# Optimization experiments

Hardware: AMD Instinct MI355X
Metric: run time of the kernel (lower is better)

Reference implementation:

```python
import math
import jax, jax.numpy as jnp
import numpy as np

N, C, T, V = 256, 128, 64, 25
OUT, H = 128, 4
D = OUT // H  # 32
MAX_LEN = 64
KSIZE = 9
EPS = 1e-5
NEG = -1e9


def setup_inputs() -> dict:
    key = jax.random.key(0)
    ks = jax.random.split(key, 20)
    std = 0.02
    return {
        "x": jax.random.normal(ks[0], (N, C, T, V), jnp.float32),
        # BatchNorm (eval mode) on input
        "bn_gamma": 1.0 + 0.1 * jax.random.normal(ks[1], (C,), jnp.float32),
        "bn_beta": 0.1 * jax.random.normal(ks[2], (C,), jnp.float32),
        "bn_mean": 0.1 * jax.random.normal(ks[3], (C,), jnp.float32),
        "bn_var": jax.random.uniform(ks[4], (C,), jnp.float32, 0.5, 1.5),
        # 1x1 convs (qkv_kernel=1)
        "qk_w": std * jax.random.normal(ks[5], (2 * OUT, C), jnp.float32),
        "qk_b": std * jax.random.normal(ks[6], (2 * OUT,), jnp.float32),
        "v_w": std * jax.random.normal(ks[7], (OUT, C), jnp.float32),
        "v_b": std * jax.random.normal(ks[8], (OUT,), jnp.float32),
        "logit_scale": jnp.full((H, 1, 1), math.log(math.sqrt(D)), jnp.float32),
        "rel_pos_bias": std * jax.random.normal(ks[9], (H, 2 * MAX_LEN - 1), jnp.float32),
        "proj_w": std * jax.random.normal(ks[10], (OUT, OUT), jnp.float32),
        "proj_b": std * jax.random.normal(ks[11], (OUT,), jnp.float32),
        # output BatchNorm (eval mode)
        "bno_gamma": 1.0 + 0.1 * jax.random.normal(ks[12], (OUT,), jnp.float32),
        "bno_beta": 0.1 * jax.random.normal(ks[13], (OUT,), jnp.float32),
        "bno_mean": 0.1 * jax.random.normal(ks[14], (OUT,), jnp.float32),
        "bno_var": jax.random.uniform(ks[15], (OUT,), jnp.float32, 0.5, 1.5),
    }


def _bn(x, gamma, beta, mean, var):
    # eval-mode BatchNorm2d over channel dim of (N, C, T, V)
    inv = gamma / jnp.sqrt(var + EPS)
    return (x - mean[:, None, None]) * inv[:, None, None] + beta[:, None, None]


def reference(x, bn_gamma, bn_beta, bn_mean, bn_var, qk_w, qk_b, v_w, v_b,
              logit_scale, rel_pos_bias, proj_w, proj_b,
              bno_gamma, bno_beta, bno_mean, bno_var):
    n, c, t, v = x.shape
    x_in = x
    xb = _bn(x, bn_gamma, bn_beta, bn_mean, bn_var)

    # 1x1 conv qk: (n, 2*OUT, t, v) -> split into q, k of shape (n, v, h, t, d)
    qk = jnp.einsum('nctv,oc->notv', xb, qk_w) + qk_b[:, None, None]
    qk = qk.reshape(n, 2, H, D, t, v).transpose(1, 0, 5, 2, 4, 3)  # (2, n, v, h, t, d)
    q, k = qk[0], qk[1]
    val = (jnp.einsum('nctv,oc->notv', xb, v_w) + v_b[:, None, None])
    val = val.reshape(n, H, D, t, v).transpose(0, 4, 1, 3, 2)  # (n, v, h, t, d)

    # cosine-sim attention: L2-normalize q, k; learned per-head temperature
    scale = jnp.exp(jnp.minimum(logit_scale, math.log(100.0)))  # (h,1,1)
    q = q / jnp.maximum(jnp.linalg.norm(q, axis=-1, keepdims=True), 1e-12) * scale
    k = k / jnp.maximum(jnp.linalg.norm(k, axis=-1, keepdims=True), 1e-12)

    # SDPA applies an extra 1/sqrt(d) scale by default
    scores = jnp.einsum('nvhid,nvhjd->nvhij', q, k) / math.sqrt(D)

    coords = jnp.arange(t)
    rel_idx = coords[None, :] - coords[:, None] + (MAX_LEN - 1)  # (t, t)
    bias = rel_pos_bias[:, rel_idx]  # (h, t, t)
    local = jnp.abs(coords[:, None] - coords[None, :]) <= KSIZE // 2  # (t, t)

    scores = jnp.where(local[None, None, None], scores + bias[None, None], NEG)
    attn = jax.nn.softmax(scores, axis=-1)
    out = jnp.einsum('nvhij,nvhjd->nvhid', attn, val)  # (n, v, h, t, d)
    out = out.transpose(0, 2, 4, 3, 1).reshape(n, OUT, t, v)

    out = jnp.einsum('nctv,oc->notv', out, proj_w) + proj_b[:, None, None] + x_in
    # stride=1 -> pool is identity; ffn_ratio=0 -> no FFN; dropout=0
    out = _bn(out, bno_gamma, bno_beta, bno_mean, bno_var)
    return out
```

## Files before the change

### kernel.cpp

```cpp
#include <hip/hip_runtime.h>
#include <hip/hip_bf16.h>

typedef __attribute__((ext_vector_type(8))) short bf16x8;
typedef __attribute__((ext_vector_type(4))) float f32x4;

static __device__ __forceinline__ unsigned short f2bf(float f){
  __hip_bfloat16 h = __float2bfloat16(f);
  return __builtin_bit_cast(unsigned short, h);
}
static __device__ __forceinline__ unsigned int pk2(float a, float b){
  return (unsigned int)f2bf(a) | ((unsigned int)f2bf(b) << 16);
}
static __device__ __forceinline__ float bf2f(unsigned short h){
  return __uint_as_float(((unsigned int)h) << 16);
}
static __device__ __forceinline__ f32x4 mfma16(bf16x8 a, bf16x8 b, f32x4 c){
  return __builtin_amdgcn_mfma_f32_16x16x32_bf16(a, b, c, 0, 0, 0);
}

__global__ void prep_kernel(
    const float* __restrict__ bn_g, const float* __restrict__ bn_b,
    const float* __restrict__ bn_m, const float* __restrict__ bn_v,
    const float* __restrict__ qk_w, const float* __restrict__ qk_b,
    const float* __restrict__ v_w,  const float* __restrict__ v_b,
    const float* __restrict__ ls,   const float* __restrict__ proj_w,
    const float* __restrict__ proj_b,
    const float* __restrict__ bo_g, const float* __restrict__ bo_b,
    const float* __restrict__ bo_m, const float* __restrict__ bo_v,
    unsigned short* __restrict__ Wqkv, unsigned short* __restrict__ Wp,
    float* __restrict__ bqf, float* __restrict__ bpf,
    float* __restrict__ rsf, float* __restrict__ shf)
{
  int g = blockIdx.x * 256 + threadIdx.x;
  if (g < 384){
    const float* wr = (g < 256) ? (qk_w + g * 128) : (v_w + (g - 256) * 128);
    float acc = (g < 256) ? qk_b[g] : v_b[g - 256];
    for (int c = 0; c < 128; c++){
      float inv = bn_g[c] * rsqrtf(bn_v[c] + 1e-5f);
      float sh  = bn_b[c] - bn_m[c] * inv;
      float wv  = wr[c];
      Wqkv[g * 128 + c] = f2bf(wv * inv);
      acc += wv * sh;
    }
    bqf[g] = acc;
  } else if (g < 512){
    int o = g - 384;
    float invo = bo_g[o] * rsqrtf(bo_v[o] + 1e-5f);
    for (int c = 0; c < 128; c++)
      Wp[o * 128 + c] = f2bf(proj_w[o * 128 + c] * invo);
    bpf[o] = (proj_b[o] - bo_m[o]) * invo + bo_b[o];
    rsf[o] = invo;
    if (o < 4)
      shf[o] = expf(fminf(ls[o], 4.6051701859880914f)) * 0.17677669529663687f;
  }
}

__global__ __launch_bounds__(256) void pack_x(const float* __restrict__ x,
                                              unsigned short* __restrict__ xb)
{
  __shared__ __align__(16) unsigned short tile[200][136];
  int n = blockIdx.x >> 3;
  int slab = blockIdx.x & 7;
  int t0 = slab * 8;
  int tid = threadIdx.x;
  const float* xn = x + (long)n * 204800 + (long)t0 * 25;
  #pragma unroll 5
  for (int k = 0; k < 25; k++){
    int idx = tid + k * 256;
    int c  = idx / 50;
    int r4 = idx - c * 50;
    float4 f = *((const float4*)(xn + (long)c * 1600 + r4 * 4));
    tile[r4*4+0][c] = f2bf(f.x);
    tile[r4*4+1][c] = f2bf(f.y);
    tile[r4*4+2][c] = f2bf(f.z);
    tile[r4*4+3][c] = f2bf(f.w);
  }
  __syncthreads();
  for (int k = 0; k < 13; k++){
    int idx = tid + k * 256;
    if (idx < 3200){
      int r  = idx >> 4;
      int u  = idx & 15;
      int lt = r / 25;
      int vv = r - lt * 25;
      int c0 = (u ^ lt) * 8;
      uint4 d = *((const uint4*)&tile[r][c0]);
      *((uint4*)(xb + ((long)(n * 25 + vv) * 64 + t0 + lt) * 128 + u * 8)) = d;
    }
  }
}

__global__ __launch_bounds__(256) void unpack_out(const unsigned short* __restrict__ ob,
                                                  float* __restrict__ out)
{
  __shared__ __align__(16) unsigned short tile[200][136];
  int n = blockIdx.x >> 3;
  int slab = blockIdx.x & 7;
  int t0 = slab * 8;
  int tid = threadIdx.x;
  for (int k = 0; k < 13; k++){
    int idx = tid + k * 256;
    if (idx < 3200){
      int r  = idx >> 4;
      int u  = idx & 15;
      int lt = r / 25;
      int vv = r - lt * 25;
      uint4 d = *((const uint4*)(ob + ((long)(n * 25 + vv) * 64 + t0 + lt) * 128 + u * 8));
      int c0 = (u ^ lt) * 8;
      *((uint4*)&tile[r][c0]) = d;
    }
  }
  __syncthreads();
  float* on = out + (long)n * 204800 + (long)t0 * 25;
  #pragma unroll 5
  for (int k = 0; k < 25; k++){
    int idx = tid + k * 256;
    int c  = idx / 50;
    int r4 = idx - c * 50;
    float4 f;
    f.x = bf2f(tile[r4*4+0][c]);
    f.y = bf2f(tile[r4*4+1][c]);
    f.z = bf2f(tile[r4*4+2][c]);
    f.w = bf2f(tile[r4*4+3][c]);
    *((float4*)(on + (long)c * 1600 + r4 * 4)) = f;
  }
}

#define B_X     0
#define B_R1    16384
#define B_VT    57344
#define B_BQ    74752
#define B_BP    76288
#define B_RS    76800
#define B_SH    77312
#define B_BIAS  77328
#define B_TOTAL 79360

__global__ __launch_bounds__(256, 2) void fused_compute(
    const unsigned short* __restrict__ xb,
    const unsigned short* __restrict__ Wqkv,
    const unsigned short* __restrict__ Wp,
    const float* __restrict__ bqf,
    const float* __restrict__ bpf,
    const float* __restrict__ rsf,
    const float* __restrict__ shf,
    const float* __restrict__ relb,
    unsigned short* __restrict__ ob)
{
  __shared__ __align__(16) char smem[B_TOTAL];
  unsigned short* xl   = (unsigned short*)(smem + B_X);
  unsigned short* r1   = (unsigned short*)(smem + B_R1);
  unsigned short* vT   = (unsigned short*)(smem + B_VT);
  float* c_bq   = (float*)(smem + B_BQ);
  float* c_bp   = (float*)(smem + B_BP);
  float* c_rs   = (float*)(smem + B_RS);
  float* c_sh   = (float*)(smem + B_SH);
  float* c_bias = (float*)(smem + B_BIAS);

  int bid = blockIdx.x;
  int swz = (bid & 7) * 800 + (bid >> 3);
  long tileoff = (long)swz * 8192;
  int tid  = threadIdx.x;
  int lane = tid & 63;
  int w    = tid >> 6;
  int h    = w;
  int l4   = lane >> 4;
  int l15  = lane & 15;

  for (int i = tid; i < 384; i += 256) c_bq[i] = bqf[i];
  if (tid < 128){ c_bp[tid] = bpf[tid]; c_rs[tid] = rsf[tid]; }
  if (tid < 4) c_sh[tid] = shf[tid];
  for (int i = tid; i < 508; i += 256) c_bias[i] = relb[i];
  {
    const uint4* src = (const uint4*)(xb + tileoff);
    uint4* dst = (uint4*)xl;
    #pragma unroll
    for (int i = 0; i < 4; i++) dst[tid + i * 256] = src[tid + i * 256];
  }
  __syncthreads();

  const f32x4 zero4 = {0.f, 0.f, 0.f, 0.f};

  unsigned short* qlds = r1 + h * 5120;
  unsigned short* klds = qlds + 2560;
  {
    int rowbase[6] = {32*h, 32*h + 16, 128 + 32*h, 128 + 32*h + 16,
                      256 + 32*h, 256 + 32*h + 16};
    f32x4 acc[6][4];
    #pragma unroll
    for (int m = 0; m < 6; m++)
      #pragma unroll
      for (int nt = 0; nt < 4; nt++) acc[m][nt] = zero4;
    #pragma unroll
    for (int ks = 0; ks < 4; ks++){
      int ko = ks * 32 + l4 * 8;
      bf16x8 a[6], b[4];
      #pragma unroll
      for (int m = 0; m < 6; m++)
        a[m] = *((const bf16x8*)(Wqkv + (rowbase[m] + l15) * 128 + ko));
      #pragma unroll
      for (int nt = 0; nt < 4; nt++){
        int row = nt * 16 + l15;
        b[nt] = *((const bf16x8*)((const char*)xl + row * 256 + ((ko * 2) ^ ((row & 7) << 4))));
      }
      #pragma unroll
      for (int m = 0; m < 6; m++)
        #pragma unroll
        for (int nt = 0; nt < 4; nt++)
          acc[m][nt] = mfma16(a[m], b[nt], acc[m][nt]);
    }
    #pragma unroll
    for (int m = 0; m < 6; m++)
      #pragma unroll
      for (int nt = 0; nt < 4; nt++)
        #pragma unroll
        for (int r = 0; r < 4; r++)
          acc[m][nt][r] += c_bq[rowbase[m] + l4 * 4 + r];

    float scq[4], sck[4];
    #pragma unroll
    for (int nt = 0; nt < 4; nt++){
      float ssq = 0.f, ssk = 0.f;
      #pragma unroll
      for (int r = 0; r < 4; r++){
        ssq += acc[0][nt][r] * acc[0][nt][r] + acc[1][nt][r] * acc[1][nt][r];
        ssk += acc[2][nt][r] * acc[2][nt][r] + acc[3][nt][r] * acc[3][nt][r];
      }
      ssq += __shfl_xor(ssq, 16); ssq += __shfl_xor(ssq, 32);
      ssk += __shfl_xor(ssk, 16); ssk += __shfl_xor(ssk, 32);
      scq[nt] = c_sh[h] / fmaxf(sqrtf(ssq), 1e-12f);
      sck[nt] = 1.0f   / fmaxf(sqrtf(ssk), 1e-12f);
    }
    #pragma unroll
    for (int m = 0; m < 2; m++)
      #pragma unroll
      for (int nt = 0; nt < 4; nt++){
        uint2 p;
        p.x = pk2(acc[m][nt][0] * scq[nt], acc[m][nt][1] * scq[nt]);
        p.y = pk2(acc[m][nt][2] * scq[nt], acc[m][nt][3] * scq[nt]);
        *((uint2*)&qlds[(nt * 16 + l15) * 40 + m * 16 + l4 * 4]) = p;
      }
    #pragma unroll
    for (int m = 2; m < 4; m++)
      #pragma unroll
      for (int nt = 0; nt < 4; nt++){
        uint2 p;
        p.x = pk2(acc[m][nt][0] * sck[nt], acc[m][nt][1] * sck[nt]);
        p.y = pk2(acc[m][nt][2] * sck[nt], acc[m][nt][3] * sck[nt]);
        *((uint2*)&klds[(nt * 16 + l15) * 40 + (m - 2) * 16 + l4 * 4]) = p;
      }
    #pragma unroll
    for (int m = 4; m < 6; m++)
      #pragma unroll
      for (int nt = 0; nt < 4; nt++)
        #pragma unroll
        for (int r = 0; r < 4; r++)
          vT[(h * 32 + (m - 4) * 16 + l4 * 4 + r) * 68 + nt * 16 + l15] = f2bf(acc[m][nt][r]);
  }
  __builtin_amdgcn_sched_barrier(0);

  bf16x8 kf[4], qf[4];
  {
    int ko = l4 * 8;
    #pragma unroll
    for (int jt = 0; jt < 4; jt++)
      kf[jt] = *((const bf16x8*)&klds[(jt * 16 + l15) * 40 + ko]);
    #pragma unroll
    for (int it = 0; it < 4; it++)
      qf[it] = *((const bf16x8*)&qlds[(it * 16 + l15) * 40 + ko]);
  }
  __builtin_amdgcn_sched_barrier(0);

  unsigned short* attn = r1 + h * 5120;
  {
    f32x4 sAcc[4][4];
    #pragma unroll
    for (int jt = 0; jt < 4; jt++)
      #pragma unroll
      for (int it = 0; it < 4; it++) sAcc[jt][it] = zero4;
    #pragma unroll
    for (int jt = 0; jt < 4; jt++)
      #pragma unroll
      for (int it = 0; it < 4; it++)
        sAcc[jt][it] = mfma16(kf[jt], qf[it], sAcc[jt][it]);

    #pragma unroll
    for (int it = 0; it < 4; it++){
      int i = it * 16 + l15;
      float sv[16];
      float mx = -1e30f;
      #pragma unroll
      for (int jt = 0; jt < 4; jt++){
        #pragma unroll
        for (int r = 0; r < 4; r++){
          int j = jt * 16 + l4 * 4 + r;
          int rel = j - i;
          float s;
          if (rel < -4 || rel > 4) s = -1e9f;
          else s = sAcc[jt][it][r] + c_bias[h * 127 + rel + 63];
          sv[jt * 4 + r] = s;
          mx = fmaxf(mx, s);
        }
      }
      mx = fmaxf(mx, __shfl_xor(mx, 16));
      mx = fmaxf(mx, __shfl_xor(mx, 32));
      float sum = 0.f;
      #pragma unroll
      for (int k2 = 0; k2 < 16; k2++){
        float p = __expf(sv[k2] - mx);
        sv[k2] = p; sum += p;
      }
      sum += __shfl_xor(sum, 16);
      sum += __shfl_xor(sum, 32);
      float rs = 1.0f / sum;
      #pragma unroll
      for (int jt = 0; jt < 4; jt++){
        uint2 p;
        p.x = pk2(sv[jt*4+0] * rs, sv[jt*4+1] * rs);
        p.y = pk2(sv[jt*4+2] * rs, sv[jt*4+3] * rs);
        *((uint2*)&attn[i * 72 + jt * 16 + l4 * 4]) = p;
      }
    }
  }
  __builtin_amdgcn_sched_barrier(0);

  bf16x8 av[2][2], bv2[4][2];
  {
    int ko = l4 * 8;
    #pragma unroll
    for (int mt = 0; mt < 2; mt++)
      #pragma unroll
      for (int ks2 = 0; ks2 < 2; ks2++)
        av[mt][ks2] = *((const bf16x8*)&vT[(h * 32 + mt * 16 + l15) * 68 + ks2 * 32 + ko]);
    #pragma unroll
    for (int it = 0; it < 4; it++)
      #pragma unroll
      for (int ks2 = 0; ks2 < 2; ks2++)
        bv2[it][ks2] = *((const bf16x8*)&attn[(it * 16 + l15) * 72 + ks2 * 32 + ko]);
  }
  __syncthreads();

  unsigned short* ao = r1;
  {
    f32x4 pAcc[2][4];
    #pragma unroll
    for (int mt = 0; mt < 2; mt++)
      #pragma unroll
      for (int it = 0; it < 4; it++) pAcc[mt][it] = zero4;
    #pragma unroll
    for (int mt = 0; mt < 2; mt++)
      #pragma unroll
      for (int it = 0; it < 4; it++)
        #pragma unroll
        for (int ks2 = 0; ks2 < 2; ks2++)
          pAcc[mt][it] = mfma16(av[mt][ks2], bv2[it][ks2], pAcc[mt][it]);
    #pragma unroll
    for (int mt = 0; mt < 2; mt++)
      #pragma unroll
      for (int it = 0; it < 4; it++){
        int d0 = mt * 16 + l4 * 4;
        int i  = it * 16 + l15;
        uint2 p;
        p.x = pk2(pAcc[mt][it][0], pAcc[mt][it][1]);
        p.y = pk2(pAcc[mt][it][2], pAcc[mt][it][3]);
        *((uint2*)&ao[i * 136 + h * 32 + d0]) = p;
      }
  }
  __syncthreads();

  {
    f32x4 acc2[2][4];
    #pragma unroll
    for (int mt = 0; mt < 2; mt++)
      #pragma unroll
      for (int nt = 0; nt < 4; nt++) acc2[mt][nt] = zero4;
    #pragma unroll
    for (int ks = 0; ks < 4; ks++){
      int ko = ks * 32 + l4 * 8;
      bf16x8 a2[2], b2[4];
      #pragma unroll
      for (int mt = 0; mt < 2; mt++)
        a2[mt] = *((const bf16x8*)(Wp + (w * 32 + mt * 16 + l15) * 128 + ko));
      #pragma unroll
      for (int nt = 0; nt < 4; nt++)
        b2[nt] = *((const bf16x8*)&ao[(nt * 16 + l15) * 136 + ko]);
      #pragma unroll
      for (int mt = 0; mt < 2; mt++)
        #pragma unroll
        for (int nt = 0; nt < 4; nt++)
          acc2[mt][nt] = mfma16(a2[mt], b2[nt], acc2[mt][nt]);
    }
    #pragma unroll
    for (int mt = 0; mt < 2; mt++)
      #pragma unroll
      for (int nt = 0; nt < 4; nt++){
        int o0 = w * 32 + mt * 16 + l4 * 4;
        int t2 = nt * 16 + l15;
        char* cell = (char*)xl + t2 * 256 + ((o0 * 2) ^ ((t2 & 7) << 4));
        uint2 resid = *((const uint2*)cell);
        float r0 = bf2f((unsigned short)(resid.x & 0xFFFFu));
        float r1f = bf2f((unsigned short)(resid.x >> 16));
        float r2 = bf2f((unsigned short)(resid.y & 0xFFFFu));
        float r3 = bf2f((unsigned short)(resid.y >> 16));
        uint2 p;
        p.x = pk2(acc2[mt][nt][0] + c_bp[o0+0] + r0 * c_rs[o0+0],
                  acc2[mt][nt][1] + c_bp[o0+1] + r1f * c_rs[o0+1]);
        p.y = pk2(acc2[mt][nt][2] + c_bp[o0+2] + r2 * c_rs[o0+2],
                  acc2[mt][nt][3] + c_bp[o0+3] + r3 * c_rs[o0+3]);
        *((uint2*)cell) = p;
      }
  }
  __syncthreads();
  {
    const uint4* sxl = (const uint4*)xl;
    uint4* obt = (uint4*)(ob + tileoff);
    #pragma unroll
    for (int i = 0; i < 4; i++) obt[tid + i * 256] = sxl[tid + i * 256];
  }
}

#define F_X     0
#define F_RB    17408
#define F_VT    58368
#define F_BQ    76800
#define F_BP    78336
#define F_RS    78848
#define F_SH    79360
#define F_BIAS  79376
#define F_TOTAL 81408

__global__ __launch_bounds__(256, 2) void fused_scatter(
    const float* __restrict__ x,
    const unsigned short* __restrict__ Wqkv,
    const unsigned short* __restrict__ Wp,
    const float* __restrict__ bqf,
    const float* __restrict__ bpf,
    const float* __restrict__ rsf,
    const float* __restrict__ shf,
    const float* __restrict__ relb,
    float* __restrict__ out)
{
  __shared__ __align__(16) char smem[F_TOTAL];
  unsigned short* xl   = (unsigned short*)(smem + F_X);
  unsigned short* rbu  = (unsigned short*)(smem + F_RB);
  unsigned short* vT   = (unsigned short*)(smem + F_VT);
  float* c_bq   = (float*)(smem + F_BQ);
  float* c_bp   = (float*)(smem + F_BP);
  float* c_rs   = (float*)(smem + F_RS);
  float* c_sh   = (float*)(smem + F_SH);
  float* c_bias = (float*)(smem + F_BIAS);

  int bid = blockIdx.x;
  int swz = (bid & 7) * 800 + (bid >> 3);
  int n = swz / 25;
  int v = swz - n * 25;
  int tid  = threadIdx.x;
  int lane = tid & 63;
  int w    = tid >> 6;
  int l4   = lane >> 4;
  int l15  = lane & 15;

  for (int i = tid; i < 384; i += 256) c_bq[i] = bqf[i];
  if (tid < 128){ c_bp[tid] = bpf[tid]; c_rs[tid] = rsf[tid]; }
  if (tid < 4) c_sh[tid] = shf[tid];
  for (int i = tid; i < 508; i += 256) c_bias[i] = relb[i];

  {
    const float* xb2 = x + (long)n * 204800 + v;
    int t  = lane;
    int cg = w * 32;
    #pragma unroll
    for (int i = 0; i < 4; i++){
      unsigned int pk[4];
      #pragma unroll
      for (int e = 0; e < 4; e++){
        int c = cg + i * 8 + e * 2;
        pk[e] = pk2(xb2[(long)c * 1600 + t * 25], xb2[(long)(c + 1) * 1600 + t * 25]);
      }
      uint4 q4; q4.x = pk[0]; q4.y = pk[1]; q4.z = pk[2]; q4.w = pk[3];
      *((uint4*)&xl[t * 136 + cg + i * 8]) = q4;
    }
  }
  __syncthreads();

  const f32x4 zero4 = {0.f, 0.f, 0.f, 0.f};

  {
    f32x4 acc[6][4];
    #pragma unroll
    for (int m = 0; m < 6; m++)
      #pragma unroll
      for (int nt = 0; nt < 4; nt++) acc[m][nt] = zero4;
    int Mb = w * 96;
    #pragma unroll
    for (int ks = 0; ks < 4; ks++){
      int ko = ks * 32 + l4 * 8;
      bf16x8 a[6], b[4];
      #pragma unroll
      for (int m = 0; m < 6; m++)
        a[m] = *((const bf16x8*)(Wqkv + (Mb + m * 16 + l15) * 128 + ko));
      #pragma unroll
      for (int nt = 0; nt < 4; nt++)
        b[nt] = *((const bf16x8*)&xl[(nt * 16 + l15) * 136 + ko]);
      #pragma unroll
      for (int m = 0; m < 6; m++)
        #pragma unroll
        for (int nt = 0; nt < 4; nt++)
          acc[m][nt] = mfma16(a[m], b[nt], acc[m][nt]);
    }
    #pragma unroll
    for (int m = 0; m < 6; m++){
      #pragma unroll
      for (int nt = 0; nt < 4; nt++){
        #pragma unroll
        for (int r = 0; r < 4; r++){
          int o  = Mb + m * 16 + l4 * 4 + r;
          int t2 = nt * 16 + l15;
          unsigned short bv = f2bf(acc[m][nt][r] + c_bq[o]);
          if (o < 256){
            rbu[(((o >> 7) * 4 + ((o >> 5) & 3)) * 64 + t2) * 40 + (o & 31)] = bv;
          } else {
            vT[(o - 256) * 72 + t2] = bv;
          }
        }
      }
    }
  }
  __syncthreads();

  {
    #pragma unroll
    for (int rr = 0; rr < 2; rr++){
      int r = tid + rr * 256;
      unsigned short* row = &rbu[r * 40];
      uint4 u0 = *((uint4*)(row + 0));
      uint4 u1 = *((uint4*)(row + 8));
      uint4 u2 = *((uint4*)(row + 16));
      uint4 u3 = *((uint4*)(row + 24));
      unsigned int uu[16] = {u0.x,u0.y,u0.z,u0.w, u1.x,u1.y,u1.z,u1.w,
                             u2.x,u2.y,u2.z,u2.w, u3.x,u3.y,u3.z,u3.w};
      float vals[32];
      float ss = 0.f;
      #pragma unroll
      for (int k2 = 0; k2 < 16; k2++){
        float f0 = bf2f((unsigned short)(uu[k2] & 0xFFFFu));
        float f1 = bf2f((unsigned short)(uu[k2] >> 16));
        vals[2*k2] = f0; vals[2*k2+1] = f1;
        ss += f0 * f0 + f1 * f1;
      }
      float sc = 1.0f / fmaxf(sqrtf(ss), 1e-12f);
      if (r < 256) sc *= c_sh[(r >> 6) & 3];
      #pragma unroll
      for (int k2 = 0; k2 < 16; k2++)
        uu[k2] = pk2(vals[2*k2] * sc, vals[2*k2+1] * sc);
      u0.x=uu[0];u0.y=uu[1];u0.z=uu[2];u0.w=uu[3];
      u1.x=uu[4];u1.y=uu[5];u1.z=uu[6];u1.w=uu[7];
      u2.x=uu[8];u2.y=uu[9];u2.z=uu[10];u2.w=uu[11];
      u3.x=uu[12];u3.y=uu[13];u3.z=uu[14];u3.w=uu[15];
      *((uint4*)(row + 0))  = u0;
      *((uint4*)(row + 8))  = u1;
      *((uint4*)(row + 16)) = u2;
      *((uint4*)(row + 24)) = u3;
    }
  }
  __syncthreads();

  int h = w;
  bf16x8 kf[4], qf[4];
  {
    const unsigned short* kb = &rbu[(256 + h * 64) * 40];
    const unsigned short* qb = &rbu[(h * 64) * 40];
    int ko = l4 * 8;
    #pragma unroll
    for (int jt = 0; jt < 4; jt++)
      kf[jt] = *((const bf16x8*)(kb + (jt * 16 + l15) * 40 + ko));
    #pragma unroll
    for (int it = 0; it < 4; it++)
      qf[it] = *((const bf16x8*)(qb + (it * 16 + l15) * 40 + ko));
  }
  __syncthreads();

  unsigned short* attn = rbu + h * 4608;
  {
    f32x4 sAcc[4][4];
    #pragma unroll
    for (int jt = 0; jt < 4; jt++)
      #pragma unroll
      for (int it = 0; it < 4; it++) sAcc[jt][it] = zero4;
    #pragma unroll
    for (int jt = 0; jt < 4; jt++)
      #pragma unroll
      for (int it = 0; it < 4; it++)
        sAcc[jt][it] = mfma16(kf[jt], qf[it], sAcc[jt][it]);

    #pragma unroll
    for (int it = 0; it < 4; it++){
      int i = it * 16 + l15;
      float sv[16];
      float mx = -1e30f;
      #pragma unroll
      for (int jt = 0; jt < 4; jt++){
        #pragma unroll
        for (int r = 0; r < 4; r++){
          int j = jt * 16 + l4 * 4 + r;
          int rel = j - i;
          float s;
          if (rel < -4 || rel > 4) s = -1e9f;
          else s = sAcc[jt][it][r] + c_bias[h * 127 + rel + 63];
          sv[jt * 4 + r] = s;
          mx = fmaxf(mx, s);
        }
      }
      mx = fmaxf(mx, __shfl_xor(mx, 16));
      mx = fmaxf(mx, __shfl_xor(mx, 32));
      float sum = 0.f;
      #pragma unroll
      for (int k2 = 0; k2 < 16; k2++){
        float p = __expf(sv[k2] - mx);
        sv[k2] = p; sum += p;
      }
      sum += __shfl_xor(sum, 16);
      sum += __shfl_xor(sum, 32);
      float rs = 1.0f / sum;
      #pragma unroll
      for (int jt = 0; jt < 4; jt++)
        #pragma unroll
        for (int r = 0; r < 4; r++)
          attn[i * 72 + (jt * 16 + l4 * 4 + r)] = f2bf(sv[jt * 4 + r] * rs);
    }
  }

  bf16x8 av[2][2], bv2[4][2];
  {
    int ko = l4 * 8;
    #pragma unroll
    for (int mt = 0; mt < 2; mt++)
      #pragma unroll
      for (int ks2 = 0; ks2 < 2; ks2++)
        av[mt][ks2] = *((const bf16x8*)&vT[(h * 32 + mt * 16 + l15) * 72 + ks2 * 32 + ko]);
    #pragma unroll
    for (int it = 0; it < 4; it++)
      #pragma unroll
      for (int ks2 = 0; ks2 < 2; ks2++)
        bv2[it][ks2] = *((const bf16x8*)&attn[(it * 16 + l15) * 72 + ks2 * 32 + ko]);
  }
  __syncthreads();

  unsigned short* ao = rbu;
  {
    f32x4 pAcc[2][4];
    #pragma unroll
    for (int mt = 0; mt < 2; mt++)
      #pragma unroll
      for (int it = 0; it < 4; it++) pAcc[mt][it] = zero4;
    #pragma unroll
    for (int mt = 0; mt < 2; mt++)
      #pragma unroll
      for (int it = 0; it < 4; it++)
        #pragma unroll
        for (int ks2 = 0; ks2 < 2; ks2++)
          pAcc[mt][it] = mfma16(av[mt][ks2], bv2[it][ks2], pAcc[mt][it]);
    #pragma unroll
    for (int mt = 0; mt < 2; mt++)
      #pragma unroll
      for (int it = 0; it < 4; it++)
        #pragma unroll
        for (int r = 0; r < 4; r++){
          int d = mt * 16 + l4 * 4 + r;
          int i = it * 16 + l15;
          ao[i * 136 + h * 32 + d] = f2bf(pAcc[mt][it][r]);
        }
  }
  __syncthreads();

  {
    f32x4 acc2[2][4];
    #pragma unroll
    for (int mt = 0; mt < 2; mt++)
      #pragma unroll
      for (int nt = 0; nt < 4; nt++) acc2[mt][nt] = zero4;
    #pragma unroll
    for (int ks = 0; ks < 4; ks++){
      int ko = ks * 32 + l4 * 8;
      bf16x8 a2[2], b2[4];
      #pragma unroll
      for (int mt = 0; mt < 2; mt++)
        a2[mt] = *((const bf16x8*)(Wp + (w * 32 + mt * 16 + l15) * 128 + ko));
      #pragma unroll
      for (int nt = 0; nt < 4; nt++)
        b2[nt] = *((const bf16x8*)&ao[(nt * 16 + l15) * 136 + ko]);
      #pragma unroll
      for (int mt = 0; mt < 2; mt++)
        #pragma unroll
        for (int nt = 0; nt < 4; nt++)
          acc2[mt][nt] = mfma16(a2[mt], b2[nt], acc2[mt][nt]);
    }
    float* outp = out + (long)n * 204800 + v;
    #pragma unroll
    for (int mt = 0; mt < 2; mt++)
      #pragma unroll
      for (int nt = 0; nt < 4; nt++)
        #pragma unroll
        for (int r = 0; r < 4; r++){
          int o  = w * 32 + mt * 16 + l4 * 4 + r;
          int t2 = nt * 16 + l15;
          float val = acc2[mt][nt][r] + c_bp[o] + bf2f(xl[t2 * 136 + o]) * c_rs[o];
          outp[(long)o * 1600 + t2 * 25] = val;
        }
  }
}

extern "C" void kernel_launch(void* const* d_in, const int* in_sizes, int n_in,
                              void* d_out, int out_size, void* d_ws, size_t ws_size,
                              hipStream_t stream)
{
  const float* x     = (const float*)d_in[0];
  const float* bn_g  = (const float*)d_in[1];
  const float* bn_b  = (const float*)d_in[2];
  const float* bn_m  = (const float*)d_in[3];
  const float* bn_v  = (const float*)d_in[4];
  const float* qk_w  = (const float*)d_in[5];
  const float* qk_b  = (const float*)d_in[6];
  const float* v_w   = (const float*)d_in[7];
  const float* v_b   = (const float*)d_in[8];
  const float* ls    = (const float*)d_in[9];
  const float* relb  = (const float*)d_in[10];
  const float* pj_w  = (const float*)d_in[11];
  const float* pj_b  = (const float*)d_in[12];
  const float* bo_g  = (const float*)d_in[13];
  const float* bo_b  = (const float*)d_in[14];
  const float* bo_m  = (const float*)d_in[15];
  const float* bo_v  = (const float*)d_in[16];

  const size_t XB_BYTES = 104857600;
  const size_t NEED = 2 * XB_BYTES + 98304 + 32768 + 1536 + 512 + 512 + 16;

  char* ws = (char*)d_ws;
  size_t wbase = (ws_size >= NEED) ? (2 * XB_BYTES) : 0;

  unsigned short* Wqkv = (unsigned short*)(ws + wbase);
  unsigned short* Wp   = (unsigned short*)(ws + wbase + 98304);
  float* bqf = (float*)(ws + wbase + 131072);
  float* bpf = (float*)(ws + wbase + 132608);
  float* rsf = (float*)(ws + wbase + 133120);
  float* shf = (float*)(ws + wbase + 133632);

  hipLaunchKernelGGL(prep_kernel, dim3(2), dim3(256), 0, stream,
                     bn_g, bn_b, bn_m, bn_v, qk_w, qk_b, v_w, v_b, ls,
                     pj_w, pj_b, bo_g, bo_b, bo_m, bo_v,
                     Wqkv, Wp, bqf, bpf, rsf, shf);

  if (ws_size >= NEED){
    unsigned short* xb = (unsigned short*)(ws);
    unsigned short* ob = (unsigned short*)(ws + XB_BYTES);
    hipLaunchKernelGGL(pack_x, dim3(2048), dim3(256), 0, stream, x, xb);
    hipLaunchKernelGGL(fused_compute, dim3(6400), dim3(256), 0, stream,
                       xb, Wqkv, Wp, bqf, bpf, rsf, shf, relb, ob);
    hipLaunchKernelGGL(unpack_out, dim3(2048), dim3(256), 0, stream, ob, (float*)d_out);
  } else {
    hipLaunchKernelGGL(fused_scatter, dim3(6400), dim3(256), 0, stream,
                       x, Wqkv, Wp, bqf, bpf, rsf, shf, relb, (float*)d_out);
  }
}
```

Measured before the change: 346.2 us.

## Split each head across two waves using 512-thread blocks in fused_compute

Doubles the block to 512 threads (8 waves), so two waves now share one head, each handling half of the 64 time-rows in the QKV projection, scores/softmax and attn·V stages. The output projection gives each wave 16 output channels instead of 32. The intra-head sched_barriers become __syncthreads, since K/Q/V now come from two waves, and the V fragment load moves earlier. The aim is more resident waves to hide latency with smaller per-wave accumulator state. The cost is extra block-wide barriers, duplicated weight-fragment loads, and a tighter register budget from __launch_bounds__(512,4), which could cause spills.

```diff
diff --git a/kernel.cpp b/kernel.cpp
--- a/kernel.cpp
+++ b/kernel.cpp
@@ -136,7 +136,7 @@
 #define B_BIAS  77328
 #define B_TOTAL 79360
 
-__global__ __launch_bounds__(256, 2) void fused_compute(
+__global__ __launch_bounds__(512, 4) void fused_compute(
     const unsigned short* __restrict__ xb,
     const unsigned short* __restrict__ Wqkv,
     const unsigned short* __restrict__ Wp,
@@ -163,19 +163,20 @@
   int tid  = threadIdx.x;
   int lane = tid & 63;
   int w    = tid >> 6;
-  int h    = w;
+  int h    = w >> 1;
+  int nb   = (w & 1) * 2;
   int l4   = lane >> 4;
   int l15  = lane & 15;
 
-  for (int i = tid; i < 384; i += 256) c_bq[i] = bqf[i];
+  if (tid < 384) c_bq[tid] = bqf[tid];
   if (tid < 128){ c_bp[tid] = bpf[tid]; c_rs[tid] = rsf[tid]; }
   if (tid < 4) c_sh[tid] = shf[tid];
-  for (int i = tid; i < 508; i += 256) c_bias[i] = relb[i];
+  for (int i = tid; i < 508; i += 512) c_bias[i] = relb[i];
   {
     const uint4* src = (const uint4*)(xb + tileoff);
     uint4* dst = (uint4*)xl;
     #pragma unroll
-    for (int i = 0; i < 4; i++) dst[tid + i * 256] = src[tid + i * 256];
+    for (int i = 0; i < 2; i++) dst[tid + i * 512] = src[tid + i * 512];
   }
   __syncthreads();
 
@@ -186,107 +187,112 @@
   {
     int rowbase[6] = {32*h, 32*h + 16, 128 + 32*h, 128 + 32*h + 16,
                       256 + 32*h, 256 + 32*h + 16};
-    f32x4 acc[6][4];
+    f32x4 acc[6][2];
     #pragma unroll
     for (int m = 0; m < 6; m++)
       #pragma unroll
-      for (int nt = 0; nt < 4; nt++) acc[m][nt] = zero4;
+      for (int q = 0; q < 2; q++) acc[m][q] = zero4;
     #pragma unroll
     for (int ks = 0; ks < 4; ks++){
       int ko = ks * 32 + l4 * 8;
-      bf16x8 a[6], b[4];
+      bf16x8 a[6], b[2];
       #pragma unroll
       for (int m = 0; m < 6; m++)
         a[m] = *((const bf16x8*)(Wqkv + (rowbase[m] + l15) * 128 + ko));
       #pragma unroll
-      for (int nt = 0; nt < 4; nt++){
-        int row = nt * 16 + l15;
-        b[nt] = *((const bf16x8*)((const char*)xl + row * 256 + ((ko * 2) ^ ((row & 7) << 4))));
+      for (int q = 0; q < 2; q++){
+        int row = (nb + q) * 16 + l15;
+        b[q] = *((const bf16x8*)((const char*)xl + row * 256 + ((ko * 2) ^ ((row & 7) << 4))));
       }
       #pragma unroll
       for (int m = 0; m < 6; m++)
         #pragma unroll
-        for (int nt = 0; nt < 4; nt++)
-          acc[m][nt] = mfma16(a[m], b[nt], acc[m][nt]);
+        for (int q = 0; q < 2; q++)
+          acc[m][q] = mfma16(a[m], b[q], acc[m][q]);
     }
     #pragma unroll
     for (int m = 0; m < 6; m++)
       #pragma unroll
-      for (int nt = 0; nt < 4; nt++)
+      for (int q = 0; q < 2; q++)
         #pragma unroll
         for (int r = 0; r < 4; r++)
-          acc[m][nt][r] += c_bq[rowbase[m] + l4 * 4 + r];
-
-    float scq[4], sck[4];
-    #pragma unroll
-    for (int nt = 0; nt < 4; nt++){
+          acc[m][q][r] += c_bq[rowbase[m] + l4 * 4 + r];
+
+    float scq[2], sck[2];
+    #pragma unroll
+    for (int q = 0; q < 2; q++){
       float ssq = 0.f, ssk = 0.f;
       #pragma unroll
       for (int r = 0; r < 4; r++){
-        ssq += acc[0][nt][r] * acc[0][nt][r] + acc[1][nt][r] * acc[1][nt][r];
-        ssk += acc[2][nt][r] * acc[2][nt][r] + acc[3][nt][r] * acc[3][nt][r];
+        ssq += acc[0][q][r] * acc[0][q][r] + acc[1][q][r] * acc[1][q][r];
+        ssk += acc[2][q][r] * acc[2][q][r] + acc[3][q][r] * acc[3][q][r];
       }
       ssq += __shfl_xor(ssq, 16); ssq += __shfl_xor(ssq, 32);
       ssk += __shfl_xor(ssk, 16); ssk += __shfl_xor(ssk, 32);
-      scq[nt] = c_sh[h] / fmaxf(sqrtf(ssq), 1e-12f);
-      sck[nt] = 1.0f   / fmaxf(sqrtf(ssk), 1e-12f);
+      scq[q] = c_sh[h] / fmaxf(sqrtf(ssq), 1e-12f);
+      sck[q] = 1.0f   / fmaxf(sqrtf(ssk), 1e-12f);
     }
     #pragma unroll
     for (int m = 0; m < 2; m++)
       #pragma unroll
-      for (int nt = 0; nt < 4; nt++){
+      for (int q = 0; q < 2; q++){
         uint2 p;
-        p.x = pk2(acc[m][nt][0] * scq[nt], acc[m][nt][1] * scq[nt]);
-        p.y = pk2(acc[m][nt][2] * scq[nt], acc[m][nt][3] * scq[nt]);
-        *((uint2*)&qlds[(nt * 16 + l15) * 40 + m * 16 + l4 * 4]) = p;
+        p.x = pk2(acc[m][q][0] * scq[q], acc[m][q][1] * scq[q]);
+        p.y = pk2(acc[m][q][2] * scq[q], acc[m][q][3] * scq[q]);
+        *((uint2*)&qlds[((nb + q) * 16 + l15) * 40 + m * 16 + l4 * 4]) = p;
       }
     #pragma unroll
     for (int m = 2; m < 4; m++)
       #pragma unroll
-      for (int nt = 0; nt < 4; nt++){
+      for (int q = 0; q < 2; q++){
         uint2 p;
-        p.x = pk2(acc[m][nt][0] * sck[nt], acc[m][nt][1] * sck[nt]);
-        p.y = pk2(acc[m][nt][2] * sck[nt], acc[m][nt][3] * sck[nt]);
-        *((uint2*)&klds[(nt * 16 + l15) * 40 + (m - 2) * 16 + l4 * 4]) = p;
+        p.x = pk2(acc[m][q][0] * sck[q], acc[m][q][1] * sck[q]);
+        p.y = pk2(acc[m][q][2] * sck[q], acc[m][q][3] * sck[q]);
+        *((uint2*)&klds[((nb + q) * 16 + l15) * 40 + (m - 2) * 16 + l4 * 4]) = p;
       }
     #pragma unroll
     for (int m = 4; m < 6; m++)
       #pragma unroll
-      for (int nt = 0; nt < 4; nt++)
+      for (int q = 0; q < 2; q++)
         #pragma unroll
         for (int r = 0; r < 4; r++)
-          vT[(h * 32 + (m - 4) * 16 + l4 * 4 + r) * 68 + nt * 16 + l15] = f2bf(acc[m][nt][r]);
-  }
-  __builtin_amdgcn_sched_barrier(0);
-
-  bf16x8 kf[4], qf[4];
+          vT[(h * 32 + (m - 4) * 16 + l4 * 4 + r) * 68 + (nb + q) * 16 + l15] = f2bf(acc[m][q][r]);
+  }
+  __syncthreads();
+
+  bf16x8 kf[4], qf[2], av[2][2];
   {
     int ko = l4 * 8;
     #pragma unroll
     for (int jt = 0; jt < 4; jt++)
       kf[jt] = *((const bf16x8*)&klds[(jt * 16 + l15) * 40 + ko]);
     #pragma unroll
-    for (int it = 0; it < 4; it++)
-      qf[it] = *((const bf16x8*)&qlds[(it * 16 + l15) * 40 + ko]);
-  }
-  __builtin_amdgcn_sched_barrier(0);
+    for (int q = 0; q < 2; q++)
+      qf[q] = *((const bf16x8*)&qlds[((nb + q) * 16 + l15) * 40 + ko]);
+    #pragma unroll
+    for (int mt = 0; mt < 2; mt++)
+      #pragma unroll
+      for (int ks2 = 0; ks2 < 2; ks2++)
+        av[mt][ks2] = *((const bf16x8*)&vT[(h * 32 + mt * 16 + l15) * 68 + ks2 * 32 + ko]);
+  }
+  __syncthreads();
 
   unsigned short* attn = r1 + h * 5120;
   {
-    f32x4 sAcc[4][4];
+    f32x4 sAcc[4][2];
     #pragma unroll
     for (int jt = 0; jt < 4; jt++)
       #pragma unroll
-      for (int it = 0; it < 4; it++) sAcc[jt][it] = zero4;
+      for (int q = 0; q < 2; q++) sAcc[jt][q] = zero4;
     #pragma unroll
     for (int jt = 0; jt < 4; jt++)
       #pragma unroll
-      for (int it = 0; it < 4; it++)
-        sAcc[jt][it] = mfma16(kf[jt], qf[it], sAcc[jt][it]);
-
-    #pragma unroll
-    for (int it = 0; it < 4; it++){
-      int i = it * 16 + l15;
+      for (int q = 0; q < 2; q++)
+        sAcc[jt][q] = mfma16(kf[jt], qf[q], sAcc[jt][q]);
+
+    #pragma unroll
+    for (int q = 0; q < 2; q++){
+      int i = (nb + q) * 16 + l15;
       float sv[16];
       float mx = -1e30f;
       #pragma unroll
@@ -297,7 +303,7 @@
           int rel = j - i;
           float s;
           if (rel < -4 || rel > 4) s = -1e9f;
-          else s = sAcc[jt][it][r] + c_bias[h * 127 + rel + 63];
+          else s = sAcc[jt][q][r] + c_bias[h * 127 + rel + 63];
           sv[jt * 4 + r] = s;
           mx = fmaxf(mx, s);
         }
@@ -324,98 +330,83 @@
   }
   __builtin_amdgcn_sched_barrier(0);
 
-  bf16x8 av[2][2], bv2[4][2];
+  bf16x8 bv2[2][2];
   {
     int ko = l4 * 8;
     #pragma unroll
-    for (int mt = 0; mt < 2; mt++)
+    for (int q = 0; q < 2; q++)
       #pragma unroll
       for (int ks2 = 0; ks2 < 2; ks2++)
-        av[mt][ks2] = *((const bf16x8*)&vT[(h * 32 + mt * 16 + l15) * 68 + ks2 * 32 + ko]);
-    #pragma unroll
-    for (int it = 0; it < 4; it++)
-      #pragma unroll
-      for (int ks2 = 0; ks2 < 2; ks2++)
-        bv2[it][ks2] = *((const bf16x8*)&attn[(it * 16 + l15) * 72 + ks2 * 32 + ko]);
+        bv2[q][ks2] = *((const bf16x8*)&attn[((nb + q) * 16 + l15) * 72 + ks2 * 32 + ko]);
   }
   __syncthreads();
 
   unsigned short* ao = r1;
   {
-    f32x4 pAcc[2][4];
-    #pragma unroll
-    for (int mt = 0; mt < 2; mt++)
-      #pragma unroll
-      for (int it = 0; it < 4; it++) pAcc[mt][it] = zero4;
-    #pragma unroll
-    for (int mt = 0; mt < 2; mt++)
-      #pragma unroll
-      for (int it = 0; it < 4; it++)
+    f32x4 pAcc[2][2];
+    #pragma unroll
+    for (int mt = 0; mt < 2; mt++)
+      #pragma unroll
+      for (int q = 0; q < 2; q++) pAcc[mt][q] = zero4;
+    #pragma unroll
+    for (int mt = 0; mt < 2; mt++)
+      #pragma unroll
+      for (int q = 0; q < 2; q++)
         #pragma unroll
         for (int ks2 = 0; ks2 < 2; ks2++)
-          pAcc[mt][it] = mfma16(av[mt][ks2], bv2[it][ks2], pAcc[mt][it]);
-    #pragma unroll
-    for (int mt = 0; mt < 2; mt++)
-      #pragma unroll
-      for (int it = 0; it < 4; it++){
+          pAcc[mt][q] = mfma16(av[mt][ks2], bv2[q][ks2], pAcc[mt][q]);
+    #pragma unroll
+    for (int mt = 0; mt < 2; mt++)
+      #pragma unroll
+      for (int q = 0; q < 2; q++){
         int d0 = mt * 16 + l4 * 4;
-        int i  = it * 16 + l15;
+        int i  = (nb + q) * 16 + l15;
         uint2 p;
-        p.x = pk2(pAcc[mt][it][0], pAcc[mt][it][1]);
-        p.y = pk2(pAcc[mt][it][2], pAcc[mt][it][3]);
+        p.x = pk2(pAcc[mt][q][0], pAcc[mt][q][1]);
+        p.y = pk2(pAcc[mt][q][2], pAcc[mt][q][3]);
         *((uint2*)&ao[i * 136 + h * 32 + d0]) = p;
       }
   }
   __syncthreads();
 
   {
-    f32x4 acc2[2][4];
-    #pragma unroll
-    for (int mt = 0; mt < 2; mt++)
-      #pragma unroll
-      for (int nt = 0; nt < 4; nt++) acc2[mt][nt] = zero4;
+    f32x4 acc2[4];
+    #pragma unroll
+    for (int nt = 0; nt < 4; nt++) acc2[nt] = zero4;
     #pragma unroll
     for (int ks = 0; ks < 4; ks++){
       int ko = ks * 32 + l4 * 8;
-      bf16x8 a2[2], b2[4];
-      #pragma unroll
-      for (int mt = 0; mt < 2; mt++)
-        a2[mt] = *((const bf16x8*)(Wp + (w * 32 + mt * 16 + l15) * 128 + ko));
-      #pragma unroll
-      for (int nt = 0; nt < 4; nt++)
-        b2[nt] = *((const bf16x8*)&ao[(nt * 16 + l15) * 136 + ko]);
-      #pragma unroll
-      for (int mt = 0; mt < 2; mt++)
-        #pragma unroll
-        for (int nt = 0; nt < 4; nt++)
-          acc2[mt][nt] = mfma16(a2[mt], b2[nt], acc2[mt][nt]);
-    }
-    #pragma unroll
-    for (int mt = 0; mt < 2; mt++)
+      bf16x8 a2 = *((const bf16x8*)(Wp + (w * 16 + l15) * 128 + ko));
       #pragma unroll
       for (int nt = 0; nt < 4; nt++){
-        int o0 = w * 32 + mt * 16 + l4 * 4;
-        int t2 = nt * 16 + l15;
-        char* cell = (char*)xl + t2 * 256 + ((o0 * 2) ^ ((t2 & 7) << 4));
-        uint2 resid = *((const uint2*)cell);
-        float r0 = bf2f((unsigned short)(resid.x & 0xFFFFu));
-        float r1f = bf2f((unsigned short)(resid.x >> 16));
-        float r2 = bf2f((unsigned short)(resid.y & 0xFFFFu));
-        float r3 = bf2f((unsigned short)(resid.y >> 16));
-        uint2 p;
-        p.x = pk2(acc2[mt][nt][0] + c_bp[o0+0] + r0 * c_rs[o0+0],
-                  acc2[mt][nt][1] + c_bp[o0+1] + r1f * c_rs[o0+1]);
-        p.y = pk2(acc2[mt][nt][2] + c_bp[o0+2] + r2 * c_rs[o0+2],
-                  acc2[mt][nt][3] + c_bp[o0+3] + r3 * c_rs[o0+3]);
-        *((uint2*)cell) = p;
-      }
+        bf16x8 b2 = *((const bf16x8*)&ao[(nt * 16 + l15) * 136 + ko]);
+        acc2[nt] = mfma16(a2, b2, acc2[nt]);
+      }
+    }
+    #pragma unroll
+    for (int nt = 0; nt < 4; nt++){
+      int o0 = w * 16 + l4 * 4;
+      int t2 = nt * 16 + l15;
+      char* cell = (char*)xl + t2 * 256 + ((o0 * 2) ^ ((t2 & 7) << 4));
+      uint2 resid = *((const uint2*)cell);
+      float r0 = bf2f((unsigned short)(resid.x & 0xFFFFu));
+      float r1f = bf2f((unsigned short)(resid.x >> 16));
+      float r2 = bf2f((unsigned short)(resid.y & 0xFFFFu));
+      float r3 = bf2f((unsigned short)(resid.y >> 16));
+      uint2 p;
+      p.x = pk2(acc2[nt][0] + c_bp[o0+0] + r0 * c_rs[o0+0],
+                acc2[nt][1] + c_bp[o0+1] + r1f * c_rs[o0+1]);
+      p.y = pk2(acc2[nt][2] + c_bp[o0+2] + r2 * c_rs[o0+2],
+                acc2[nt][3] + c_bp[o0+3] + r3 * c_rs[o0+3]);
+      *((uint2*)cell) = p;
+    }
   }
   __syncthreads();
   {
     const uint4* sxl = (const uint4*)xl;
     uint4* obt = (uint4*)(ob + tileoff);
     #pragma unroll
-    for (int i = 0; i < 4; i++) obt[tid + i * 256] = sxl[tid + i * 256];
+    for (int i = 0; i < 2; i++) obt[tid + i * 512] = sxl[tid + i * 512];
   }
 }
 
@@ -754,7 +745,7 @@
     unsigned short* xb = (unsigned short*)(ws);
     unsigned short* ob = (unsigned short*)(ws + XB_BYTES);
     hipLaunchKernelGGL(pack_x, dim3(2048), dim3(256), 0, stream, x, xb);
-    hipLaunchKernelGGL(fused_compute, dim3(6400), dim3(256), 0, stream,
+    hipLaunchKernelGGL(fused_compute, dim3(6400), dim3(512), 0, stream,
                        xb, Wqkv, Wp, bqf, bpf, rsf, shf, relb, ob);
     hipLaunchKernelGGL(unpack_out, dim3(2048), dim3(256), 0, stream, ob, (float*)d_out);
   } else {
```

Result: slower. 389.9 us (+12.6%).

## Shrink fused_compute LDS footprint with buffer aliasing and XOR swizzle for 3 blocks/CU

Applied to the files above, without the earlier changes.

Reworks the shared-memory plan of fused_compute. The x tile region is reused for the transposed V once the residual values have been read into registers, and each head's Q/K/attention data now sits in an 8 KB region laid out with an XOR swizzle instead of padded rows. LDS per block drops from about 79 KB to about 54 KB, and launch bounds go from 2 to 3 blocks per CU to raise occupancy. In exchange, the residual is kept in registers across the whole kernel and an extra barrier is added, which raises register pressure and may cause spills under the tighter 3-block limit.

```diff
diff --git a/kernel.cpp b/kernel.cpp
--- a/kernel.cpp
+++ b/kernel.cpp
@@ -126,17 +126,16 @@
   }
 }
 
-#define B_X     0
-#define B_R1    16384
-#define B_VT    57344
-#define B_BQ    74752
-#define B_BP    76288
-#define B_RS    76800
-#define B_SH    77312
-#define B_BIAS  77328
-#define B_TOTAL 79360
-
-__global__ __launch_bounds__(256, 2) void fused_compute(
+#define B_RA    0
+#define B_RB    16384
+#define B_BQ    49152
+#define B_BP    50688
+#define B_RS    51200
+#define B_SH    51712
+#define B_BIAS  51728
+#define B_TOTAL 53760
+
+__global__ __launch_bounds__(256, 3) void fused_compute(
     const unsigned short* __restrict__ xb,
     const unsigned short* __restrict__ Wqkv,
     const unsigned short* __restrict__ Wp,
@@ -148,9 +147,7 @@
     unsigned short* __restrict__ ob)
 {
   __shared__ __align__(16) char smem[B_TOTAL];
-  unsigned short* xl   = (unsigned short*)(smem + B_X);
-  unsigned short* r1   = (unsigned short*)(smem + B_R1);
-  unsigned short* vT   = (unsigned short*)(smem + B_VT);
+  char* ra = smem + B_RA;
   float* c_bq   = (float*)(smem + B_BQ);
   float* c_bp   = (float*)(smem + B_BP);
   float* c_rs   = (float*)(smem + B_RS);
@@ -167,22 +164,23 @@
   int l4   = lane >> 4;
   int l15  = lane & 15;
 
+  char* qkh = smem + B_RB + h * 8192;
+
   for (int i = tid; i < 384; i += 256) c_bq[i] = bqf[i];
   if (tid < 128){ c_bp[tid] = bpf[tid]; c_rs[tid] = rsf[tid]; }
   if (tid < 4) c_sh[tid] = shf[tid];
   for (int i = tid; i < 508; i += 256) c_bias[i] = relb[i];
   {
     const uint4* src = (const uint4*)(xb + tileoff);
-    uint4* dst = (uint4*)xl;
+    uint4* dst = (uint4*)ra;
     #pragma unroll
     for (int i = 0; i < 4; i++) dst[tid + i * 256] = src[tid + i * 256];
   }
   __syncthreads();
 
   const f32x4 zero4 = {0.f, 0.f, 0.f, 0.f};
-
-  unsigned short* qlds = r1 + h * 5120;
-  unsigned short* klds = qlds + 2560;
+  uint2 resid[2][4];
+
   {
     int rowbase[6] = {32*h, 32*h + 16, 128 + 32*h, 128 + 32*h + 16,
                       256 + 32*h, 256 + 32*h + 16};
@@ -201,7 +199,7 @@
       #pragma unroll
       for (int nt = 0; nt < 4; nt++){
         int row = nt * 16 + l15;
-        b[nt] = *((const bf16x8*)((const char*)xl + row * 256 + ((ko * 2) ^ ((row & 7) << 4))));
+        b[nt] = *((const bf16x8*)(ra + row * 256 + ((ko * 2) ^ ((row & 7) << 4))));
       }
       #pragma unroll
       for (int m = 0; m < 6; m++)
@@ -209,6 +207,16 @@
         for (int nt = 0; nt < 4; nt++)
           acc[m][nt] = mfma16(a[m], b[nt], acc[m][nt]);
     }
+    #pragma unroll
+    for (int mt = 0; mt < 2; mt++)
+      #pragma unroll
+      for (int nt = 0; nt < 4; nt++){
+        int o0 = w * 32 + mt * 16 + l4 * 4;
+        int t2 = nt * 16 + l15;
+        resid[mt][nt] = *((const uint2*)(ra + t2 * 256 + ((o0 * 2) ^ ((t2 & 7) << 4))));
+      }
+    __syncthreads();
+
     #pragma unroll
     for (int m = 0; m < 6; m++)
       #pragma unroll
@@ -235,43 +243,50 @@
     for (int m = 0; m < 2; m++)
       #pragma unroll
       for (int nt = 0; nt < 4; nt++){
+        int row = nt * 16 + l15;
         uint2 p;
         p.x = pk2(acc[m][nt][0] * scq[nt], acc[m][nt][1] * scq[nt]);
         p.y = pk2(acc[m][nt][2] * scq[nt], acc[m][nt][3] * scq[nt]);
-        *((uint2*)&qlds[(nt * 16 + l15) * 40 + m * 16 + l4 * 4]) = p;
+        *((uint2*)(qkh + row * 128 + ((m * 32 + l4 * 8) ^ ((row & 7) << 4)))) = p;
       }
     #pragma unroll
     for (int m = 2; m < 4; m++)
       #pragma unroll
       for (int nt = 0; nt < 4; nt++){
+        int row = nt * 16 + l15;
         uint2 p;
         p.x = pk2(acc[m][nt][0] * sck[nt], acc[m][nt][1] * sck[nt]);
         p.y = pk2(acc[m][nt][2] * sck[nt], acc[m][nt][3] * sck[nt]);
-        *((uint2*)&klds[(nt * 16 + l15) * 40 + (m - 2) * 16 + l4 * 4]) = p;
+        *((uint2*)(qkh + row * 128 + ((64 + (m - 2) * 32 + l4 * 8) ^ ((row & 7) << 4)))) = p;
       }
     #pragma unroll
     for (int m = 4; m < 6; m++)
       #pragma unroll
       for (int nt = 0; nt < 4; nt++)
         #pragma unroll
-        for (int r = 0; r < 4; r++)
-          vT[(h * 32 + (m - 4) * 16 + l4 * 4 + r) * 68 + nt * 16 + l15] = f2bf(acc[m][nt][r]);
+        for (int r = 0; r < 4; r++){
+          int d = h * 32 + (m - 4) * 16 + l4 * 4 + r;
+          *((unsigned short*)(ra + d * 128 + ((((nt * 16 + l15) * 2)) ^ ((d & 7) << 4)))) =
+            f2bf(acc[m][nt][r]);
+        }
   }
   __builtin_amdgcn_sched_barrier(0);
 
   bf16x8 kf[4], qf[4];
   {
-    int ko = l4 * 8;
-    #pragma unroll
-    for (int jt = 0; jt < 4; jt++)
-      kf[jt] = *((const bf16x8*)&klds[(jt * 16 + l15) * 40 + ko]);
-    #pragma unroll
-    for (int it = 0; it < 4; it++)
-      qf[it] = *((const bf16x8*)&qlds[(it * 16 + l15) * 40 + ko]);
+    #pragma unroll
+    for (int jt = 0; jt < 4; jt++){
+      int row = jt * 16 + l15;
+      kf[jt] = *((const bf16x8*)(qkh + row * 128 + ((64 + l4 * 16) ^ ((row & 7) << 4))));
+    }
+    #pragma unroll
+    for (int it = 0; it < 4; it++){
+      int row = it * 16 + l15;
+      qf[it] = *((const bf16x8*)(qkh + row * 128 + ((l4 * 16) ^ ((row & 7) << 4))));
+    }
   }
   __builtin_amdgcn_sched_barrier(0);
 
-  unsigned short* attn = r1 + h * 5120;
   {
     f32x4 sAcc[4][4];
     #pragma unroll
@@ -318,7 +333,7 @@
         uint2 p;
         p.x = pk2(sv[jt*4+0] * rs, sv[jt*4+1] * rs);
         p.y = pk2(sv[jt*4+2] * rs, sv[jt*4+3] * rs);
-        *((uint2*)&attn[i * 72 + jt * 16 + l4 * 4]) = p;
+        *((uint2*)(qkh + i * 128 + ((jt * 32 + l4 * 8) ^ ((i & 7) << 4)))) = p;
       }
     }
   }
@@ -326,21 +341,24 @@
 
   bf16x8 av[2][2], bv2[4][2];
   {
-    int ko = l4 * 8;
-    #pragma unroll
-    for (int mt = 0; mt < 2; mt++)
-      #pragma unroll
-      for (int ks2 = 0; ks2 < 2; ks2++)
-        av[mt][ks2] = *((const bf16x8*)&vT[(h * 32 + mt * 16 + l15) * 68 + ks2 * 32 + ko]);
+    #pragma unroll
+    for (int mt = 0; mt < 2; mt++)
+      #pragma unroll
+      for (int ks2 = 0; ks2 < 2; ks2++){
+        int row = h * 32 + mt * 16 + l15;
+        av[mt][ks2] = *((const bf16x8*)(ra + row * 128 + ((ks2 * 64 + l4 * 16) ^ ((row & 7) << 4))));
+      }
     #pragma unroll
     for (int it = 0; it < 4; it++)
       #pragma unroll
-      for (int ks2 = 0; ks2 < 2; ks2++)
-        bv2[it][ks2] = *((const bf16x8*)&attn[(it * 16 + l15) * 72 + ks2 * 32 + ko]);
-  }
-  __syncthreads();
-
-  unsigned short* ao = r1;
+      for (int ks2 = 0; ks2 < 2; ks2++){
+        int row = it * 16 + l15;
+        bv2[it][ks2] = *((const bf16x8*)(qkh + row * 128 + ((ks2 * 64 + l4 * 16) ^ ((row & 7) << 4))));
+      }
+  }
+  __syncthreads();
+
+  unsigned short* ao = (unsigned short*)(smem + B_RB);
   {
     f32x4 pAcc[2][4];
     #pragma unroll
@@ -396,23 +414,22 @@
       for (int nt = 0; nt < 4; nt++){
         int o0 = w * 32 + mt * 16 + l4 * 4;
         int t2 = nt * 16 + l15;
-        char* cell = (char*)xl + t2 * 256 + ((o0 * 2) ^ ((t2 & 7) << 4));
-        uint2 resid = *((const uint2*)cell);
-        float r0 = bf2f((unsigned short)(resid.x & 0xFFFFu));
-        float r1f = bf2f((unsigned short)(resid.x >> 16));
-        float r2 = bf2f((unsigned short)(resid.y & 0xFFFFu));
-        float r3 = bf2f((unsigned short)(resid.y >> 16));
+        uint2 rd = resid[mt][nt];
+        float r0 = bf2f((unsigned short)(rd.x & 0xFFFFu));
+        float r1f = bf2f((unsigned short)(rd.x >> 16));
+        float r2 = bf2f((unsigned short)(rd.y & 0xFFFFu));
+        float r3 = bf2f((unsigned short)(rd.y >> 16));
         uint2 p;
         p.x = pk2(acc2[mt][nt][0] + c_bp[o0+0] + r0 * c_rs[o0+0],
                   acc2[mt][nt][1] + c_bp[o0+1] + r1f * c_rs[o0+1]);
         p.y = pk2(acc2[mt][nt][2] + c_bp[o0+2] + r2 * c_rs[o0+2],
                   acc2[mt][nt][3] + c_bp[o0+3] + r3 * c_rs[o0+3]);
-        *((uint2*)cell) = p;
-      }
-  }
-  __syncthreads();
-  {
-    const uint4* sxl = (const uint4*)xl;
+        *((uint2*)(ra + t2 * 256 + ((o0 * 2) ^ ((t2 & 7) << 4)))) = p;
+      }
+  }
+  __syncthreads();
+  {
+    const uint4* sxl = (const uint4*)ra;
     uint4* obt = (uint4*)(ob + tileoff);
     #pragma unroll
     for (int i = 0; i < 4; i++) obt[tid + i * 256] = sxl[tid + i * 256];
```

Result: slower. 361.6 us (+4.5%).
